# Kernel optimization log

Hardware: AMD Instinct MI355X
Metric: run time of the kernel (lower is better)

## Reference

```python
import jax, jax.numpy as jnp
import numpy as np
import math

B, Q_LEN, K_LEN = 8, 512, 512
D_MODEL, H = 512, 8
DK = D_MODEL // H


def setup_inputs() -> dict:
    key = jax.random.key(0)
    ks = jax.random.split(key, 12)
    inp = {
        "query": jax.random.normal(ks[0], (B, Q_LEN, D_MODEL), jnp.float32),
        "key": jax.random.normal(ks[1], (B, K_LEN, D_MODEL), jnp.float32),
        "value": jax.random.normal(ks[2], (B, K_LEN, D_MODEL), jnp.float32),
        "relative_embeddings": jax.random.normal(ks[3], (K_LEN, Q_LEN, D_MODEL), jnp.float32),
        # causal mask: 1 = attend, 0 = masked
        "mask": jnp.tril(jnp.ones((Q_LEN, K_LEN), dtype=bool)),
        "Wq": jax.random.normal(ks[4], (D_MODEL, D_MODEL), jnp.float32) / math.sqrt(D_MODEL),
        "Wk": jax.random.normal(ks[5], (D_MODEL, D_MODEL), jnp.float32) / math.sqrt(D_MODEL),
        "Wv": jax.random.normal(ks[6], (D_MODEL, D_MODEL), jnp.float32) / math.sqrt(D_MODEL),
        "Wo": jax.random.normal(ks[7], (D_MODEL, D_MODEL), jnp.float32) / math.sqrt(D_MODEL),
        "Wr": jax.random.normal(ks[8], (D_MODEL, D_MODEL), jnp.float32) / math.sqrt(D_MODEL),
        "u": jax.random.normal(ks[9], (H, DK), jnp.float32),
        "v": jax.random.normal(ks[10], (H, DK), jnp.float32),
    }
    return inp


def reference(query, key, value, relative_embeddings, mask, Wq, Wk, Wv, Wo, Wr, u, v):
    b, q_len, d_model = query.shape
    k_len = key.shape[1]
    # torch nn.Linear(x) = x @ W.T (bias=False)
    Qh = (query @ Wq.T).reshape(b, q_len, H, DK).transpose(0, 2, 1, 3)   # bhqd
    Kh = (key @ Wk.T).reshape(b, k_len, H, DK).transpose(0, 2, 1, 3)     # bhkd
    Vh = (value @ Wv.T).reshape(b, k_len, H, DK).transpose(0, 2, 1, 3)   # bhkd
    # relative position projection: (k_len, q_len, d_model)
    R = relative_embeddings @ Wr.T
    # view(k,q,H,dk).permute(2,1,0,3) -> (H, q, k, dk)
    Rh = R.reshape(k_len, q_len, H, DK).transpose(2, 1, 0, 3)
    # content score: (Q + u) K^T
    content = jnp.einsum("bhqd,bhkd->bhqk", Qh + u[None, :, None, :], Kh)
    # position score: (Q + v) R^T, R per-head per-query
    position = jnp.einsum("bhqd,hqkd->bhqk", Qh + v[None, :, None, :], Rh)
    scores = (content + position) / math.sqrt(DK)
    scores = jnp.where(mask[None, None, :, :], scores, -1e9)
    weights = jax.nn.softmax(scores, axis=-1)  # dropout is identity in eval
    out = jnp.einsum("bhqk,bhkd->bhqd", weights, Vh)
    out = out.transpose(0, 2, 1, 3).reshape(b, q_len, d_model)
    out = out @ Wo.T
    return (out, weights)
```

## Files before the change

kernel.cpp:

```cpp
#include <hip/hip_runtime.h>

#define BATCH   8
#define SEQ     512
#define DMODEL  512
#define NHEAD   8
#define DKH     64

typedef __attribute__((ext_vector_type(8))) short bf16x8;
typedef __attribute__((ext_vector_type(4))) float f32x4;

__device__ __forceinline__ short f2bf(float f) {
    union { float f; unsigned u; } v; v.f = f;
    unsigned r = v.u + 0x7FFFu + ((v.u >> 16) & 1u);
    return (short)(r >> 16);
}

#define LDK 40

__device__ __forceinline__ void stage_f32(const float* __restrict__ base,
                                          int rstride, short* lds, int tid) {
    int r = tid >> 2, c = (tid & 3) << 3;
    const float* p = base + (size_t)r * rstride + c;
    float4 x = *(const float4*)p;
    float4 y = *(const float4*)(p + 4);
    union { short s[8]; bf16x8 v; } o;
    o.s[0] = f2bf(x.x); o.s[1] = f2bf(x.y); o.s[2] = f2bf(x.z); o.s[3] = f2bf(x.w);
    o.s[4] = f2bf(y.x); o.s[5] = f2bf(y.y); o.s[6] = f2bf(y.z); o.s[7] = f2bf(y.w);
    *(bf16x8*)(lds + r * LDK + c) = o.v;
}

__device__ __forceinline__ void stage_bf16(const short* __restrict__ base,
                                           int rstride, short* lds, int tid) {
    int r = tid >> 2, c = (tid & 3) << 3;
    bf16x8 v = *(const bf16x8*)(base + (size_t)r * rstride + c);
    *(bf16x8*)(lds + r * LDK + c) = v;
}

__device__ __forceinline__ void mma_tile(const short* As, const short* Bs,
                                         int lane, int wm, int wn, f32x4 acc[2][2]) {
    int lo = lane & 15, hi = lane >> 4;
    bf16x8 a0 = *(const bf16x8*)(As + (wm * 32 + lo) * LDK + hi * 8);
    bf16x8 a1 = *(const bf16x8*)(As + (wm * 32 + 16 + lo) * LDK + hi * 8);
    bf16x8 b0 = *(const bf16x8*)(Bs + (wn * 32 + lo) * LDK + hi * 8);
    bf16x8 b1 = *(const bf16x8*)(Bs + (wn * 32 + 16 + lo) * LDK + hi * 8);
    acc[0][0] = __builtin_amdgcn_mfma_f32_16x16x32_bf16(a0, b0, acc[0][0], 0, 0, 0);
    acc[0][1] = __builtin_amdgcn_mfma_f32_16x16x32_bf16(a0, b1, acc[0][1], 0, 0, 0);
    acc[1][0] = __builtin_amdgcn_mfma_f32_16x16x32_bf16(a1, b0, acc[1][0], 0, 0, 0);
    acc[1][1] = __builtin_amdgcn_mfma_f32_16x16x32_bf16(a1, b1, acc[1][1], 0, 0, 0);
}

__global__ __launch_bounds__(256) void wrt_kernel(const float* __restrict__ Wr,
                                                  short* __restrict__ Wrt) {
    int idx = blockIdx.x * 256 + threadIdx.x;
    int n = idx >> 9, m = idx & 511;
    Wrt[idx] = f2bf(Wr[(size_t)m * 512 + n]);
}

__global__ __launch_bounds__(256) void qkv_kernel(
        const float* __restrict__ query, const float* __restrict__ key_,
        const float* __restrict__ value,
        const float* __restrict__ Wq, const float* __restrict__ Wk,
        const float* __restrict__ Wv,
        const float* __restrict__ uvec, const float* __restrict__ vvec,
        short* __restrict__ Qu, short* __restrict__ Qv,
        short* __restrict__ Kh, short* __restrict__ Vt) {
    __shared__ short As[64 * LDK], Bs[64 * LDK];
    int f = blockIdx.x;
    int i = f >> 3;
    int nt = i & 7;
    int gm = (f & 7) * 24 + (i >> 3);
    int mode = gm >> 6, mt = gm & 63;
    const float* x = mode == 0 ? query : (mode == 1 ? key_ : value);
    const float* W = mode == 0 ? Wq : (mode == 1 ? Wk : Wv);
    int tid = threadIdx.x, lane = tid & 63, w = tid >> 6, wm = w >> 1, wn = w & 1;
    const float* Abase = x + (size_t)mt * 64 * DMODEL;
    const float* Bbase = W + (size_t)nt * 64 * DMODEL;
    f32x4 acc[2][2] = {};
    for (int kt = 0; kt < DMODEL; kt += 32) {
        __syncthreads();
        stage_f32(Abase + kt, DMODEL, As, tid);
        stage_f32(Bbase + kt, DMODEL, Bs, tid);
        __syncthreads();
        mma_tile(As, Bs, lane, wm, wn, acc);
    }
    int lo = lane & 15, hi = lane >> 4;
    for (int fm = 0; fm < 2; fm++)
        for (int fn = 0; fn < 2; fn++)
            for (int r = 0; r < 4; r++) {
                int m = mt * 64 + wm * 32 + fm * 16 + hi * 4 + r;
                int n = nt * 64 + wn * 32 + fn * 16 + lo;
                float val = acc[fm][fn][r];
                int b = m >> 9, s = m & 511, h = n >> 6, d = n & 63;
                if (mode == 0) {
                    size_t idx = ((size_t)(b * NHEAD + h) * SEQ + s) * DKH + d;
                    Qu[idx] = f2bf(val + uvec[n]);
                    Qv[idx] = f2bf(val + vvec[n]);
                } else if (mode == 1) {
                    Kh[((size_t)(b * NHEAD + h) * SEQ + s) * DKH + d] = f2bf(val);
                } else {
                    Vt[((size_t)(b * NHEAD + h) * DKH + d) * SEQ + s] = f2bf(val);
                }
            }
}

__global__ __launch_bounds__(256) void t_kernel(const short* __restrict__ Qv,
                                                const short* __restrict__ Wrt,
                                                short* __restrict__ T) {
    __shared__ short As[64 * LDK], Bs[64 * LDK];
    int f = blockIdx.x;
    int i = f >> 3;
    int nt = i & 7;
    int mh = (f & 7) * 64 + (i >> 3);
    int mt = mh >> 3, h = mh & 7;
    int tid = threadIdx.x, lane = tid & 63, w = tid >> 6, wm = w >> 1, wn = w & 1;
    int m0 = mt * 64, b = m0 >> 9, q0 = m0 & 511;
    const short* Abase = Qv + ((size_t)(b * NHEAD + h) * SEQ + q0) * DKH;
    const short* Bbase = Wrt + (size_t)nt * 64 * DMODEL + h * DKH;
    f32x4 acc[2][2] = {};
    for (int kt = 0; kt < DKH; kt += 32) {
        __syncthreads();
        stage_bf16(Abase + kt, DKH, As, tid);
        stage_bf16(Bbase + kt, DMODEL, Bs, tid);
        __syncthreads();
        mma_tile(As, Bs, lane, wm, wn, acc);
    }
    int lo = lane & 15, hi = lane >> 4;
    for (int fm = 0; fm < 2; fm++)
        for (int fn = 0; fn < 2; fn++)
            for (int r = 0; r < 4; r++) {
                int q = q0 + wm * 32 + fm * 16 + hi * 4 + r;
                int n = nt * 64 + wn * 32 + fn * 16 + lo;
                T[((size_t)(b * NHEAD + h) * SEQ + q) * DMODEL + n] = f2bf(acc[fm][fn][r]);
            }
}

__global__ __launch_bounds__(256) void content_kernel(const short* __restrict__ Qu,
                                                      const short* __restrict__ Kh,
                                                      float* __restrict__ scores) {
    int f = blockIdx.x;
    int i = f >> 3;
    int bh = (f & 7) * 8 + (i >> 6);
    int rest = i & 63;
    int kt_ = rest & 7, qt = rest >> 3;
    if (kt_ > qt) return;
    __shared__ short As[64 * LDK], Bs[64 * LDK];
    int tid = threadIdx.x, lane = tid & 63, w = tid >> 6, wm = w >> 1, wn = w & 1;
    const short* Abase = Qu + ((size_t)bh * SEQ + qt * 64) * DKH;
    const short* Bbase = Kh + ((size_t)bh * SEQ + kt_ * 64) * DKH;
    f32x4 acc[2][2] = {};
    for (int kt = 0; kt < DKH; kt += 32) {
        __syncthreads();
        stage_bf16(Abase + kt, DKH, As, tid);
        stage_bf16(Bbase + kt, DKH, Bs, tid);
        __syncthreads();
        mma_tile(As, Bs, lane, wm, wn, acc);
    }
    int lo = lane & 15, hi = lane >> 4;
    for (int fm = 0; fm < 2; fm++)
        for (int fn = 0; fn < 2; fn++)
            for (int r = 0; r < 4; r++) {
                int q = qt * 64 + wm * 32 + fm * 16 + hi * 4 + r;
                int k = kt_ * 64 + wn * 32 + fn * 16 + lo;
                scores[((size_t)bh * SEQ + q) * SEQ + k] = acc[fm][fn][r];
            }
}

__global__ __launch_bounds__(256) void position_kernel(const short* __restrict__ T,
                                                       const float* __restrict__ rel,
                                                       float* __restrict__ scores) {
    int bk = blockIdx.x;
    int q = (bk & 7) * 64 + ((bk >> 3) >> 2);
    int stripe = (bk >> 3) & 3;
    if (stripe * 128 > q) return;
    __shared__ short Tl[64 * 256];
    int tid = threadIdx.x, w = tid >> 6, lane = tid & 63;
    int kbase = stripe * 128 + w * 32;
    bool active = (kbase <= q);
    int lo = lane & 15, hi = lane >> 4;
    const short* Tq = T + (size_t)q * DMODEL;
    const float* relq = rel + ((size_t)kbase * SEQ + q) * DMODEL;
    f32x4 acc[4][2] = {};
    for (int half = 0; half < 2; ++half) {
        int nbase = half * 256;
        __syncthreads();
        #pragma unroll
        for (int it = 0; it < 8; ++it) {
            int r = it * 8 + w * 2 + (lane >> 5);
            int cc = lane & 31;
            bf16x8 v = *(const bf16x8*)(Tq + (size_t)r * (SEQ * DMODEL) + nbase + cc * 8);
            int g = cc ^ (r & 7);
            *(bf16x8*)(Tl + r * 256 + g * 8) = v;
        }
        __syncthreads();
        if (active) {
            for (int nn = 0; nn < 256; nn += 32) {
                bf16x8 a[4];
                #pragma unroll
                for (int fm = 0; fm < 4; fm++) {
                    int rr = fm * 16 + lo;
                    int g = ((nn >> 3) + hi) ^ (rr & 7);
                    a[fm] = *(const bf16x8*)(Tl + rr * 256 + g * 8);
                }
                bf16x8 bfrag[2];
                #pragma unroll
                for (int fk = 0; fk < 2; fk++) {
                    const float* p = relq + (size_t)(fk * 16 + lo) * (SEQ * DMODEL)
                                   + nbase + nn + hi * 8;
                    float4 x = *(const float4*)p;
                    float4 y = *(const float4*)(p + 4);
                    union { short s[8]; bf16x8 v; } o;
                    o.s[0] = f2bf(x.x); o.s[1] = f2bf(x.y); o.s[2] = f2bf(x.z); o.s[3] = f2bf(x.w);
                    o.s[4] = f2bf(y.x); o.s[5] = f2bf(y.y); o.s[6] = f2bf(y.z); o.s[7] = f2bf(y.w);
                    bfrag[fk] = o.v;
                }
                #pragma unroll
                for (int fm = 0; fm < 4; fm++) {
                    acc[fm][0] = __builtin_amdgcn_mfma_f32_16x16x32_bf16(a[fm], bfrag[0], acc[fm][0], 0, 0, 0);
                    acc[fm][1] = __builtin_amdgcn_mfma_f32_16x16x32_bf16(a[fm], bfrag[1], acc[fm][1], 0, 0, 0);
                }
            }
        }
    }
    if (!active) return;
    #pragma unroll
    for (int fm = 0; fm < 4; fm++)
        #pragma unroll
        for (int fk = 0; fk < 2; fk++)
            #pragma unroll
            for (int r = 0; r < 4; r++) {
                int bh = fm * 16 + hi * 4 + r;
                int k = kbase + fk * 16 + lo;
                scores[((size_t)bh * SEQ + q) * SEQ + k] += acc[fm][fk][r];
            }
}

__global__ __launch_bounds__(256) void pv_sm_kernel(float* __restrict__ scores,
                                                    const short* __restrict__ Vt,
                                                    short* __restrict__ attn) {
    __shared__ short As[64 * LDK], Bs[64 * LDK];
    int f = blockIdx.x;
    int i = f >> 3;
    int bh = (f & 7) * 8 + (i >> 3);
    int qt = i & 7;
    int tid = threadIdx.x, lane = tid & 63, w = tid >> 6, wm = w >> 1, wn = w & 1;
    int kmax = (qt + 1) * 64;
    int r = tid >> 2, c4 = tid & 3;
    int q = qt * 64 + r;
    float* row = scores + ((size_t)bh * SEQ + q) * SEQ;
    float M = -1e30f, S = 0.f;
    int kbeg = c4 * 128;
    int kend = (kbeg + 128 < kmax) ? kbeg + 128 : kmax;
    for (int k = kbeg; k < kend; k += 4) {
        float4 vv = *(const float4*)(row + k);
        float x0 = (k + 0 <= q) ? vv.x * 0.125f : -1e30f;
        float x1 = (k + 1 <= q) ? vv.y * 0.125f : -1e30f;
        float x2 = (k + 2 <= q) ? vv.z * 0.125f : -1e30f;
        float x3 = (k + 3 <= q) ? vv.w * 0.125f : -1e30f;
        float mx = fmaxf(fmaxf(x0, x1), fmaxf(x2, x3));
        float Mn = fmaxf(M, mx);
        S = S * __expf(M - Mn) + __expf(x0 - Mn) + __expf(x1 - Mn)
          + __expf(x2 - Mn) + __expf(x3 - Mn);
        M = Mn;
    }
    #pragma unroll
    for (int off = 1; off <= 2; off <<= 1) {
        float Mo = __shfl_xor(M, off), So = __shfl_xor(S, off);
        float Mn = fmaxf(M, Mo);
        S = S * __expf(M - Mn) + So * __expf(Mo - Mn);
        M = Mn;
    }
    float invS = 1.0f / S;
    const short* Bbase = Vt + (size_t)bh * DKH * SEQ;
    f32x4 acc[2][2] = {};
    int cc = c4 * 8;
    for (int kt = 0; kt < SEQ; kt += 32) {
        if (kt < kmax) {
            __syncthreads();
            stage_bf16(Bbase + kt, SEQ, Bs, tid);
            float4 x = *(const float4*)(row + kt + cc);
            float4 y = *(const float4*)(row + kt + cc + 4);
            float p0 = (kt + cc + 0 <= q) ? __expf(x.x * 0.125f - M) * invS : 0.f;
            float p1 = (kt + cc + 1 <= q) ? __expf(x.y * 0.125f - M) * invS : 0.f;
            float p2 = (kt + cc + 2 <= q) ? __expf(x.z * 0.125f - M) * invS : 0.f;
            float p3 = (kt + cc + 3 <= q) ? __expf(x.w * 0.125f - M) * invS : 0.f;
            float p4 = (kt + cc + 4 <= q) ? __expf(y.x * 0.125f - M) * invS : 0.f;
            float p5 = (kt + cc + 5 <= q) ? __expf(y.y * 0.125f - M) * invS : 0.f;
            float p6 = (kt + cc + 6 <= q) ? __expf(y.z * 0.125f - M) * invS : 0.f;
            float p7 = (kt + cc + 7 <= q) ? __expf(y.w * 0.125f - M) * invS : 0.f;
            *(float4*)(row + kt + cc) = make_float4(p0, p1, p2, p3);
            *(float4*)(row + kt + cc + 4) = make_float4(p4, p5, p6, p7);
            union { short s[8]; bf16x8 v; } o;
            o.s[0] = f2bf(p0); o.s[1] = f2bf(p1); o.s[2] = f2bf(p2); o.s[3] = f2bf(p3);
            o.s[4] = f2bf(p4); o.s[5] = f2bf(p5); o.s[6] = f2bf(p6); o.s[7] = f2bf(p7);
            *(bf16x8*)(As + r * LDK + cc) = o.v;
            __syncthreads();
            mma_tile(As, Bs, lane, wm, wn, acc);
        } else {
            float4 z = make_float4(0.f, 0.f, 0.f, 0.f);
            *(float4*)(row + kt + cc) = z;
            *(float4*)(row + kt + cc + 4) = z;
        }
    }
    int lo = lane & 15, hi = lane >> 4;
    int b = bh >> 3, h = bh & 7;
    for (int fm = 0; fm < 2; fm++)
        for (int fn = 0; fn < 2; fn++)
            for (int rr = 0; rr < 4; rr++) {
                int qq = qt * 64 + wm * 32 + fm * 16 + hi * 4 + rr;
                int d = wn * 32 + fn * 16 + lo;
                attn[((size_t)b * SEQ + qq) * DMODEL + h * DKH + d] = f2bf(acc[fm][fn][rr]);
            }
}

__global__ __launch_bounds__(256) void oproj_kernel(const short* __restrict__ attn,
                                                    const float* __restrict__ Wo,
                                                    float* __restrict__ out) {
    __shared__ short As[64 * LDK], Bs[64 * LDK];
    int f = blockIdx.x;
    int i = f >> 3;
    int mt = (f & 7) * 8 + (i >> 3);
    int nt = i & 7;
    int tid = threadIdx.x, lane = tid & 63, w = tid >> 6, wm = w >> 1, wn = w & 1;
    const short* Abase = attn + (size_t)mt * 64 * DMODEL;
    const float* Bbase = Wo + (size_t)nt * 64 * DMODEL;
    f32x4 acc[2][2] = {};
    for (int kt = 0; kt < DMODEL; kt += 32) {
        __syncthreads();
        stage_bf16(Abase + kt, DMODEL, As, tid);
        stage_f32(Bbase + kt, DMODEL, Bs, tid);
        __syncthreads();
        mma_tile(As, Bs, lane, wm, wn, acc);
    }
    int lo = lane & 15, hi = lane >> 4;
    for (int fm = 0; fm < 2; fm++)
        for (int fn = 0; fn < 2; fn++)
            for (int r = 0; r < 4; r++) {
                int m = mt * 64 + wm * 32 + fm * 16 + hi * 4 + r;
                int n = nt * 64 + wn * 32 + fn * 16 + lo;
                out[(size_t)m * DMODEL + n] = acc[fm][fn][r];
            }
}

extern "C" void kernel_launch(void* const* d_in, const int* in_sizes, int n_in,
                              void* d_out, int out_size, void* d_ws, size_t ws_size,
                              hipStream_t stream) {
    (void)in_sizes; (void)n_in; (void)out_size; (void)ws_size;
    const float* query = (const float*)d_in[0];
    const float* key   = (const float*)d_in[1];
    const float* value = (const float*)d_in[2];
    const float* rel   = (const float*)d_in[3];
    const float* Wq = (const float*)d_in[5];
    const float* Wk = (const float*)d_in[6];
    const float* Wv = (const float*)d_in[7];
    const float* Wo = (const float*)d_in[8];
    const float* Wr = (const float*)d_in[9];
    const float* u  = (const float*)d_in[10];
    const float* v  = (const float*)d_in[11];

    float* out     = (float*)d_out;
    float* weights = out + (size_t)BATCH * SEQ * DMODEL;

    char* ws = (char*)d_ws;
    short* Qu   = (short*)(ws);
    short* Qv   = (short*)(ws + ((size_t)4 << 20));
    short* Kh   = (short*)(ws + ((size_t)8 << 20));
    short* Vt   = (short*)(ws + ((size_t)12 << 20));
    short* T    = (short*)(ws + ((size_t)16 << 20));
    short* attn = (short*)(ws + ((size_t)48 << 20));
    short* Wrt  = (short*)(ws + ((size_t)52 << 20));

    wrt_kernel<<<1024, 256, 0, stream>>>(Wr, Wrt);
    qkv_kernel<<<1536, 256, 0, stream>>>(query, key, value, Wq, Wk, Wv,
                                         u, v, Qu, Qv, Kh, Vt);
    t_kernel<<<4096, 256, 0, stream>>>(Qv, Wrt, T);
    content_kernel<<<4096, 256, 0, stream>>>(Qu, Kh, weights);
    position_kernel<<<2048, 256, 0, stream>>>(T, rel, weights);
    pv_sm_kernel<<<512, 256, 0, stream>>>(weights, Vt, attn);
    oproj_kernel<<<512, 256, 0, stream>>>(attn, Wo, out);
}
```

Measured before the change: 230.1 us.

## Fold Wr transpose into QKV kernel and relayout T for contiguous position staging

Merges the Wr transpose/convert into the QKV projection launch as extra blocks, which removes one kernel launch. T is stored q-major (q, bh, n), so each position block stages its 64x512 T slab in one contiguous load instead of two strided half-loads. The position kernel moves to 512-thread blocks covering a 256-wide k half with the full 512-wide reduction, which halves the block count and drops the second staging pass. The trade-off is 64KB of LDS per block, which may lower occupancy.

```diff
diff --git a/kernel.cpp b/kernel.cpp
--- a/kernel.cpp
+++ b/kernel.cpp
@@ -13,6 +13,10 @@
     union { float f; unsigned u; } v; v.f = f;
     unsigned r = v.u + 0x7FFFu + ((v.u >> 16) & 1u);
     return (short)(r >> 16);
+}
+__device__ __forceinline__ float bf2f(short s) {
+    union { unsigned u; float f; } v; v.u = ((unsigned)(unsigned short)s) << 16;
+    return v.f;
 }
 
 #define LDK 40
@@ -49,30 +53,34 @@
     acc[1][1] = __builtin_amdgcn_mfma_f32_16x16x32_bf16(a1, b1, acc[1][1], 0, 0, 0);
 }
 
-__global__ __launch_bounds__(256) void wrt_kernel(const float* __restrict__ Wr,
-                                                  short* __restrict__ Wrt) {
-    int idx = blockIdx.x * 256 + threadIdx.x;
-    int n = idx >> 9, m = idx & 511;
-    Wrt[idx] = f2bf(Wr[(size_t)m * 512 + n]);
-}
-
-__global__ __launch_bounds__(256) void qkv_kernel(
+__global__ __launch_bounds__(256) void qkvw_kernel(
         const float* __restrict__ query, const float* __restrict__ key_,
         const float* __restrict__ value,
         const float* __restrict__ Wq, const float* __restrict__ Wk,
-        const float* __restrict__ Wv,
+        const float* __restrict__ Wv, const float* __restrict__ Wr,
         const float* __restrict__ uvec, const float* __restrict__ vvec,
         short* __restrict__ Qu, short* __restrict__ Qv,
-        short* __restrict__ Kh, short* __restrict__ Vt) {
-    __shared__ short As[64 * LDK], Bs[64 * LDK];
-    int f = blockIdx.x;
+        short* __restrict__ Kh, short* __restrict__ Vt,
+        short* __restrict__ Wrt) {
+    __shared__ short As[64 * LDK], Bs[64 * LDK];
+    int f = blockIdx.x, tid = threadIdx.x;
+    if (f >= 1536) {
+        int base = (f - 1536) * 1024;
+        #pragma unroll
+        for (int j = 0; j < 4; j++) {
+            int idx = base + j * 256 + tid;
+            int n = idx >> 9, m = idx & 511;
+            Wrt[idx] = f2bf(Wr[(size_t)m * 512 + n]);
+        }
+        return;
+    }
     int i = f >> 3;
     int nt = i & 7;
     int gm = (f & 7) * 24 + (i >> 3);
     int mode = gm >> 6, mt = gm & 63;
     const float* x = mode == 0 ? query : (mode == 1 ? key_ : value);
     const float* W = mode == 0 ? Wq : (mode == 1 ? Wk : Wv);
-    int tid = threadIdx.x, lane = tid & 63, w = tid >> 6, wm = w >> 1, wn = w & 1;
+    int lane = tid & 63, w = tid >> 6, wm = w >> 1, wn = w & 1;
     const float* Abase = x + (size_t)mt * 64 * DMODEL;
     const float* Bbase = W + (size_t)nt * 64 * DMODEL;
     f32x4 acc[2][2] = {};
@@ -105,7 +113,7 @@
 
 __global__ __launch_bounds__(256) void t_kernel(const short* __restrict__ Qv,
                                                 const short* __restrict__ Wrt,
-                                                short* __restrict__ T) {
+                                                short* __restrict__ T2) {
     __shared__ short As[64 * LDK], Bs[64 * LDK];
     int f = blockIdx.x;
     int i = f >> 3;
@@ -125,12 +133,13 @@
         mma_tile(As, Bs, lane, wm, wn, acc);
     }
     int lo = lane & 15, hi = lane >> 4;
+    int bh = b * NHEAD + h;
     for (int fm = 0; fm < 2; fm++)
         for (int fn = 0; fn < 2; fn++)
             for (int r = 0; r < 4; r++) {
                 int q = q0 + wm * 32 + fm * 16 + hi * 4 + r;
                 int n = nt * 64 + wn * 32 + fn * 16 + lo;
-                T[((size_t)(b * NHEAD + h) * SEQ + q) * DMODEL + n] = f2bf(acc[fm][fn][r]);
+                T2[((size_t)q * 64 + bh) * DMODEL + n] = f2bf(acc[fm][fn][r]);
             }
 }
 
@@ -165,63 +174,55 @@
             }
 }
 
-__global__ __launch_bounds__(256) void position_kernel(const short* __restrict__ T,
+__global__ __launch_bounds__(512) void position_kernel(const short* __restrict__ T2,
                                                        const float* __restrict__ rel,
                                                        float* __restrict__ scores) {
     int bk = blockIdx.x;
-    int q = (bk & 7) * 64 + ((bk >> 3) >> 2);
-    int stripe = (bk >> 3) & 3;
-    if (stripe * 128 > q) return;
-    __shared__ short Tl[64 * 256];
+    int j = bk >> 3;
+    int q = (bk & 7) * 64 + (j >> 1);
+    int half = j & 1;
+    if (half * 256 > q) return;
+    __shared__ short Tl[64 * 512];
     int tid = threadIdx.x, w = tid >> 6, lane = tid & 63;
-    int kbase = stripe * 128 + w * 32;
-    bool active = (kbase <= q);
-    int lo = lane & 15, hi = lane >> 4;
-    const short* Tq = T + (size_t)q * DMODEL;
+    const short* Tq = T2 + (size_t)q * (64 * DMODEL);
+    #pragma unroll
+    for (int it = 0; it < 8; ++it) {
+        int chunk = it * 512 + tid;
+        int r = chunk >> 6, c = chunk & 63;
+        bf16x8 v = *(const bf16x8*)(Tq + (size_t)chunk * 8);
+        *(bf16x8*)(Tl + r * 512 + (c ^ (r & 7)) * 8) = v;
+    }
+    __syncthreads();
+    int kbase = half * 256 + w * 32;
+    if (kbase > q) return;
+    int lo = lane & 15, hi = lane >> 4;
     const float* relq = rel + ((size_t)kbase * SEQ + q) * DMODEL;
     f32x4 acc[4][2] = {};
-    for (int half = 0; half < 2; ++half) {
-        int nbase = half * 256;
-        __syncthreads();
-        #pragma unroll
-        for (int it = 0; it < 8; ++it) {
-            int r = it * 8 + w * 2 + (lane >> 5);
-            int cc = lane & 31;
-            bf16x8 v = *(const bf16x8*)(Tq + (size_t)r * (SEQ * DMODEL) + nbase + cc * 8);
-            int g = cc ^ (r & 7);
-            *(bf16x8*)(Tl + r * 256 + g * 8) = v;
-        }
-        __syncthreads();
-        if (active) {
-            for (int nn = 0; nn < 256; nn += 32) {
-                bf16x8 a[4];
-                #pragma unroll
-                for (int fm = 0; fm < 4; fm++) {
-                    int rr = fm * 16 + lo;
-                    int g = ((nn >> 3) + hi) ^ (rr & 7);
-                    a[fm] = *(const bf16x8*)(Tl + rr * 256 + g * 8);
-                }
-                bf16x8 bfrag[2];
-                #pragma unroll
-                for (int fk = 0; fk < 2; fk++) {
-                    const float* p = relq + (size_t)(fk * 16 + lo) * (SEQ * DMODEL)
-                                   + nbase + nn + hi * 8;
-                    float4 x = *(const float4*)p;
-                    float4 y = *(const float4*)(p + 4);
-                    union { short s[8]; bf16x8 v; } o;
-                    o.s[0] = f2bf(x.x); o.s[1] = f2bf(x.y); o.s[2] = f2bf(x.z); o.s[3] = f2bf(x.w);
-                    o.s[4] = f2bf(y.x); o.s[5] = f2bf(y.y); o.s[6] = f2bf(y.z); o.s[7] = f2bf(y.w);
-                    bfrag[fk] = o.v;
-                }
-                #pragma unroll
-                for (int fm = 0; fm < 4; fm++) {
-                    acc[fm][0] = __builtin_amdgcn_mfma_f32_16x16x32_bf16(a[fm], bfrag[0], acc[fm][0], 0, 0, 0);
-                    acc[fm][1] = __builtin_amdgcn_mfma_f32_16x16x32_bf16(a[fm], bfrag[1], acc[fm][1], 0, 0, 0);
-                }
-            }
-        }
-    }
-    if (!active) return;
+    for (int n = 0; n < DMODEL; n += 32) {
+        bf16x8 a[4];
+        #pragma unroll
+        for (int fm = 0; fm < 4; fm++) {
+            int rr = fm * 16 + lo;
+            int g = ((n >> 3) + hi) ^ (rr & 7);
+            a[fm] = *(const bf16x8*)(Tl + rr * 512 + g * 8);
+        }
+        bf16x8 bfrag[2];
+        #pragma unroll
+        for (int fk = 0; fk < 2; fk++) {
+            const float* p = relq + (size_t)(fk * 16 + lo) * (SEQ * DMODEL) + n + hi * 8;
+            float4 x = *(const float4*)p;
+            float4 y = *(const float4*)(p + 4);
+            union { short s[8]; bf16x8 v; } o;
+            o.s[0] = f2bf(x.x); o.s[1] = f2bf(x.y); o.s[2] = f2bf(x.z); o.s[3] = f2bf(x.w);
+            o.s[4] = f2bf(y.x); o.s[5] = f2bf(y.y); o.s[6] = f2bf(y.z); o.s[7] = f2bf(y.w);
+            bfrag[fk] = o.v;
+        }
+        #pragma unroll
+        for (int fm = 0; fm < 4; fm++) {
+            acc[fm][0] = __builtin_amdgcn_mfma_f32_16x16x32_bf16(a[fm], bfrag[0], acc[fm][0], 0, 0, 0);
+            acc[fm][1] = __builtin_amdgcn_mfma_f32_16x16x32_bf16(a[fm], bfrag[1], acc[fm][1], 0, 0, 0);
+        }
+    }
     #pragma unroll
     for (int fm = 0; fm < 4; fm++)
         #pragma unroll
@@ -365,16 +366,15 @@
     short* Qv   = (short*)(ws + ((size_t)4 << 20));
     short* Kh   = (short*)(ws + ((size_t)8 << 20));
     short* Vt   = (short*)(ws + ((size_t)12 << 20));
-    short* T    = (short*)(ws + ((size_t)16 << 20));
+    short* T2   = (short*)(ws + ((size_t)16 << 20));
     short* attn = (short*)(ws + ((size_t)48 << 20));
     short* Wrt  = (short*)(ws + ((size_t)52 << 20));
 
-    wrt_kernel<<<1024, 256, 0, stream>>>(Wr, Wrt);
-    qkv_kernel<<<1536, 256, 0, stream>>>(query, key, value, Wq, Wk, Wv,
-                                         u, v, Qu, Qv, Kh, Vt);
-    t_kernel<<<4096, 256, 0, stream>>>(Qv, Wrt, T);
+    qkvw_kernel<<<1792, 256, 0, stream>>>(query, key, value, Wq, Wk, Wv, Wr,
+                                          u, v, Qu, Qv, Kh, Vt, Wrt);
+    t_kernel<<<4096, 256, 0, stream>>>(Qv, Wrt, T2);
     content_kernel<<<4096, 256, 0, stream>>>(Qu, Kh, weights);
-    position_kernel<<<2048, 256, 0, stream>>>(T, rel, weights);
+    position_kernel<<<1024, 512, 0, stream>>>(T2, rel, weights);
     pv_sm_kernel<<<512, 256, 0, stream>>>(weights, Vt, attn);
     oproj_kernel<<<512, 256, 0, stream>>>(attn, Wo, out);
 }
```

After: 222.8 us. -3.2%, faster.
